# Kernel tuning notes

Hardware: AMD Instinct MI355X
Metric: run time of the kernel (lower is better)

## Reference

```python
import jax, jax.numpy as jnp
import numpy as np

EPS = 1e-5
NEG = -1e20


def layer_norm(x, gamma, beta):
    mu = jnp.mean(x, axis=-1, keepdims=True)
    var = jnp.mean(jnp.square(x - mu), axis=-1, keepdims=True)
    return (x - mu) * jax.lax.rsqrt(var + EPS) * gamma + beta


def setup_inputs() -> dict:
    key = jax.random.key(0)
    ks = jax.random.split(key, 12)
    B, S, D, H, HD = 2, 2048, 1024, 16, 64
    hid = H * HD
    inp = {
        "q": jax.random.normal(ks[0], (B, S, D), jnp.float32),
        "k": jax.random.normal(ks[1], (B, S, D), jnp.float32),
        "v": jax.random.normal(ks[2], (B, S, D), jnp.float32),
        "mask": jax.random.randint(ks[3], (B, 1, S, S), 0, 2, jnp.int32),
        "Wq": jax.random.normal(ks[4], (D, hid), jnp.float32) * (D ** -0.5),
        "bq": jnp.zeros((hid,), jnp.float32),
        "Wk": jax.random.normal(ks[5], (D, hid), jnp.float32) * (D ** -0.5),
        "bk": jnp.zeros((hid,), jnp.float32),
        "Wv": jax.random.normal(ks[6], (D, hid), jnp.float32) * (D ** -0.5),
        "bv": jnp.zeros((hid,), jnp.float32),
        "Wo": jax.random.normal(ks[7], (hid, D), jnp.float32) * (hid ** -0.5),
        "bo": jnp.zeros((D,), jnp.float32),
        "gamma": jnp.ones((D,), jnp.float32),
        "beta": jnp.zeros((D,), jnp.float32),
    }
    return inp


def reference(q, k, v, mask, Wq, bq, Wk, bk, Wv, bv, Wo, bo, gamma, beta):
    B, S, D = q.shape
    H, HD = 16, 64
    scale = HD ** -0.5
    qh = (layer_norm(q, gamma, beta) @ Wq + bq).reshape(B, S, H, HD).transpose(0, 2, 1, 3)
    kh = (layer_norm(k, gamma, beta) @ Wk + bk).reshape(B, S, H, HD).transpose(0, 2, 1, 3)
    vh = (layer_norm(v, gamma, beta) @ Wv + bv).reshape(B, S, H, HD).transpose(0, 2, 1, 3)
    dots = jnp.einsum('bhqd,bhkd->bhqk', qh, kh)  # [B,H,S,S]
    dots = jnp.where(mask == 0, NEG, dots) * scale  # mask BEFORE scale (as in source)
    attn = jax.nn.softmax(dots, axis=-1)
    out = jnp.einsum('bhqk,bhkd->bhqd', attn, vh)  # [B,H,S,HD]
    # Faithful to `out.view(B, S, -1)` on a [B,H,S,HD]-contiguous tensor: raw reshape,
    # no head transpose.
    out = out.reshape(B, S, H * HD)
    return out @ Wo + bo
```

## Files before the change

### kernel.cpp

```cpp
#include <hip/hip_runtime.h>

typedef short short8 __attribute__((ext_vector_type(8)));
typedef float f32x4 __attribute__((ext_vector_type(4)));

#define QSCALE 0.18033688011112042f

__device__ __forceinline__ unsigned short f2bf(float f) {
  unsigned u = __builtin_bit_cast(unsigned, f);
  u += 0x7fffu + ((u >> 16) & 1u);
  return (unsigned short)(u >> 16);
}

__device__ __forceinline__ void gload16(const void* g, void* l) {
  typedef __attribute__((address_space(1))) unsigned int gas;
  typedef __attribute__((address_space(3))) unsigned int las;
  __builtin_amdgcn_global_load_lds((gas*)(unsigned long long)g,
                                   (las*)(unsigned)(unsigned long long)l, 16, 0, 0);
}

__device__ __forceinline__ short8 mk8(unsigned r0, unsigned r1, unsigned r2, unsigned r3) {
  union { unsigned u[4]; short8 s; } t;
  t.u[0] = r0; t.u[1] = r1; t.u[2] = r2; t.u[3] = r3;
  return t.s;
}

#define MFMA16(a, b, c) __builtin_amdgcn_mfma_f32_16x16x32_bf16(a, b, c, 0, 0, 0)

__global__ __launch_bounds__(256) void wtrans_kernel(
    const float* __restrict__ Wq, const float* __restrict__ Wk,
    const float* __restrict__ Wv, const float* __restrict__ Wo,
    unsigned short* __restrict__ Wt) {
  const int wsel = blockIdx.z;
  const float* W = wsel == 0 ? Wq : wsel == 1 ? Wk : wsel == 2 ? Wv : Wo;
  const float wscale = (wsel == 0) ? QSCALE : 1.0f;
  unsigned short* out = Wt + (long)wsel * 1048576;
  __shared__ float lds[64][65];
  const int t = threadIdx.x;
  const int k0 = blockIdx.x * 64, n0 = blockIdx.y * 64;
#pragma unroll
  for (int i = 0; i < 4; ++i) {
    int r = (t >> 4) + i * 16, c4 = (t & 15) * 4;
    float4 vv = *(const float4*)(W + (long)(k0 + r) * 1024 + n0 + c4);
    lds[r][c4] = vv.x; lds[r][c4 + 1] = vv.y; lds[r][c4 + 2] = vv.z; lds[r][c4 + 3] = vv.w;
  }
  __syncthreads();
#pragma unroll
  for (int i = 0; i < 16; ++i) {
    int flat = t + i * 256;
    int n = flat >> 6, kk = flat & 63;
    out[(long)(n0 + n) * 1024 + k0 + kk] = f2bf(lds[kk][n] * wscale);
  }
}

__global__ __launch_bounds__(256) void maskpack_kernel(const int* __restrict__ mask,
                                                       unsigned* __restrict__ bits) {
  const long n = 8388608;
  const long stride = (long)gridDim.x * 256;
  const int lane = threadIdx.x & 63;
  for (long i = (long)blockIdx.x * 256 + threadIdx.x; i < n; i += stride) {
    unsigned long long bal = __ballot(mask[i] != 0);
    if ((lane & 31) == 0) bits[i >> 5] = (unsigned)(bal >> (lane & 32));
  }
}

__global__ __launch_bounds__(256) void ln_kernel(
    const float* __restrict__ q, const float* __restrict__ k, const float* __restrict__ v,
    const float* __restrict__ gamma, const float* __restrict__ beta,
    unsigned short* __restrict__ lnq, unsigned short* __restrict__ lnk,
    unsigned short* __restrict__ lnv) {
  const int row = blockIdx.x, which = blockIdx.y;
  const float* x = (which == 0 ? q : which == 1 ? k : v) + (long)row * 1024;
  unsigned short* y = (which == 0 ? lnq : which == 1 ? lnk : lnv) + (long)row * 1024;
  const int t = threadIdx.x, lane = t & 63, wv = t >> 6;
  float4 xv = ((const float4*)x)[t];
  float s = xv.x + xv.y + xv.z + xv.w;
  float s2 = xv.x * xv.x + xv.y * xv.y + xv.z * xv.z + xv.w * xv.w;
#pragma unroll
  for (int off = 32; off > 0; off >>= 1) {
    s += __shfl_down(s, off);
    s2 += __shfl_down(s2, off);
  }
  __shared__ float red[8];
  if (lane == 0) { red[wv] = s; red[wv + 4] = s2; }
  __syncthreads();
  float tot = red[0] + red[1] + red[2] + red[3];
  float tot2 = red[4] + red[5] + red[6] + red[7];
  float mu = tot * (1.0f / 1024.0f);
  float var = tot2 * (1.0f / 1024.0f) - mu * mu;
  float rs = rsqrtf(var + 1e-5f);
  float4 g = ((const float4*)gamma)[t];
  float4 be = ((const float4*)beta)[t];
  ushort4 o;
  o.x = f2bf((xv.x - mu) * rs * g.x + be.x);
  o.y = f2bf((xv.y - mu) * rs * g.y + be.y);
  o.z = f2bf((xv.z - mu) * rs * g.z + be.z);
  o.w = f2bf((xv.w - mu) * rs * g.w + be.w);
  ((ushort4*)y)[t] = o;
}

template <int BM, int MODE>
__global__ __launch_bounds__(256) void gemm_kernel(
    const unsigned short* __restrict__ A0, const unsigned short* __restrict__ A1,
    const unsigned short* __restrict__ A2, const unsigned short* __restrict__ Wt,
    const float* __restrict__ b0, const float* __restrict__ b1,
    const float* __restrict__ b2, unsigned short* __restrict__ outB,
    unsigned short* __restrict__ outV, float* __restrict__ outF) {
  constexpr int BK = 64;
  constexpr int MI = BM / 32;
  const int z = blockIdx.z;
  const unsigned short* A = z == 0 ? A0 : z == 1 ? A1 : A2;
  const unsigned short* Bt = Wt + (long)z * 1048576;
  const float* bias = z == 0 ? b0 : z == 1 ? b1 : b2;
  unsigned short* outz = outB + (long)z * 4194304;
  const float bscale = (MODE == 0 && z == 0) ? QSCALE : 1.0f;

  __shared__ char lds[BM * 128 + 16384];
  char* As = lds;
  char* Bs = lds + BM * 128;
  const int tid = threadIdx.x, lane = tid & 63, w = tid >> 6;
  const int wr = w >> 1, wc = w & 1;
  const int m0 = blockIdx.x * BM, n0 = blockIdx.y * 128;
  constexpr int K = 1024;
  constexpr int ACH = BM * 8 / 256;

  f32x4 acc[MI][4] = {};
  for (int kt = 0; kt < K / BK; ++kt) {
    __syncthreads();
#pragma unroll
    for (int i = 0; i < ACH; ++i) {
      int c = tid + i * 256;
      int row = c >> 3, pg = (c & 7) ^ (row & 7);
      gload16(A + (long)(m0 + row) * K + kt * BK + pg * 8, As + c * 16);
    }
#pragma unroll
    for (int i = 0; i < 4; ++i) {
      int c = tid + i * 256;
      int row = c >> 3, pg = (c & 7) ^ (row & 7);
      gload16(Bt + (long)(n0 + row) * K + kt * BK + pg * 8, Bs + c * 16);
    }
    asm volatile("s_waitcnt vmcnt(0)" ::: "memory");
    __syncthreads();
#pragma unroll
    for (int ks = 0; ks < 2; ++ks) {
      short8 af[MI], bf[4];
#pragma unroll
      for (int mi = 0; mi < MI; ++mi) {
        int row = wr * (BM / 2) + mi * 16 + (lane & 15);
        int part = (ks * 4 + (lane >> 4)) ^ (row & 7);
        af[mi] = *(const short8*)(As + row * 128 + part * 16);
      }
#pragma unroll
      for (int ni = 0; ni < 4; ++ni) {
        int row = wc * 64 + ni * 16 + (lane & 15);
        int part = (ks * 4 + (lane >> 4)) ^ (row & 7);
        bf[ni] = *(const short8*)(Bs + row * 128 + part * 16);
      }
#pragma unroll
      for (int mi = 0; mi < MI; ++mi)
#pragma unroll
        for (int ni = 0; ni < 4; ++ni)
          acc[mi][ni] = MFMA16(af[mi], bf[ni], acc[mi][ni]);
    }
  }
#pragma unroll
  for (int mi = 0; mi < MI; ++mi) {
    int mbase = m0 + wr * (BM / 2) + mi * 16 + ((lane >> 4) << 2);
#pragma unroll
    for (int ni = 0; ni < 4; ++ni) {
      int j = n0 + wc * 64 + ni * 16 + (lane & 15);
      float bj = bias[j] * bscale;
      float t0 = acc[mi][ni][0] + bj;
      float t1 = acc[mi][ni][1] + bj;
      float t2 = acc[mi][ni][2] + bj;
      float t3 = acc[mi][ni][3] + bj;
      if constexpr (MODE == 0) {
        int b = mbase >> 11, s = mbase & 2047;
        int h = j >> 6, d = j & 63;
        if (z == 2) {
          unsigned lo, hi;
          asm("v_cvt_pk_bf16_f32 %0, %1, %2" : "=v"(lo) : "v"(t0), "v"(t1));
          asm("v_cvt_pk_bf16_f32 %0, %1, %2" : "=v"(hi) : "v"(t2), "v"(t3));
          uint2 o; o.x = lo; o.y = hi;
          int sp = (s & ~31) | (((s >> 2) & 3) << 3) | (((s >> 4) & 1) << 2);
          *(uint2*)(outV + ((long)(b * 16 + h) * 64 + d) * 2048 + sp) = o;
        } else {
          long base = (((long)(b * 16 + h)) * 2048 + s) * 64 + d;
          outz[base] = f2bf(t0);
          outz[base + 64] = f2bf(t1);
          outz[base + 128] = f2bf(t2);
          outz[base + 192] = f2bf(t3);
        }
      } else {
        outF[(long)mbase * 1024 + j] = t0;
        outF[(long)(mbase + 1) * 1024 + j] = t1;
        outF[(long)(mbase + 2) * 1024 + j] = t2;
        outF[(long)(mbase + 3) * 1024 + j] = t3;
      }
    }
  }
}

__global__ __launch_bounds__(256, 4) void attn_kernel(
    const unsigned short* __restrict__ qh, const unsigned short* __restrict__ kh,
    const unsigned short* __restrict__ vt, const unsigned* __restrict__ mbits,
    unsigned short* __restrict__ O) {
  constexpr int S = 2048, NT = 32;
  __shared__ char lds[32768];
  char* Ks = lds;
  char* Vts = lds + 16384;
  const int tid = threadIdx.x, lane = tid & 63, w = tid >> 6;
  const int g = lane >> 4, c = lane & 15;

  const int flat = blockIdx.y * 32 + blockIdx.x;
  const int fl2 = (flat & 7) * 128 + (flat >> 3);
  const int qb = fl2 & 31, bh = fl2 >> 5, b = bh >> 4;
  const int kt0 = (fl2 & 3) * 8;

  const unsigned short* qp = qh + (long)bh * S * 64;
  const unsigned short* kp = kh + (long)bh * S * 64;
  const unsigned short* vp = vt + (long)bh * 64 * S;
  unsigned short* op = O + (long)bh * S * 64;
  const unsigned* mrow = mbits + (long)b * S * 64;
  const int q0 = qb * 64 + w * 16;
  const int myq = q0 + c;

  short8 bq_[2];
#pragma unroll
  for (int ds = 0; ds < 2; ++ds)
    bq_[ds] = *(const short8*)(qp + (long)myq * 64 + ds * 32 + g * 8);

  f32x4 o_acc[4] = {};
  float lpart = 0.f;

#define STAGE(KT, BUF)                                                              \
  {                                                                                 \
    _Pragma("unroll") for (int i = 0; i < 2; ++i) {                                 \
      int cc = tid + i * 256;                                                       \
      int row = cc >> 3, pg = (cc & 7) ^ (row & 7);                                 \
      gload16(kp + (long)((KT)*64 + row) * 64 + pg * 8, Ks + (BUF)*8192 + cc * 16); \
    }                                                                               \
    _Pragma("unroll") for (int i = 0; i < 2; ++i) {                                 \
      int cc = tid + i * 256;                                                       \
      int row = cc >> 3, pg = (cc & 7) ^ (row & 7);                                 \
      gload16(vp + (long)row * S + (KT)*64 + pg * 8, Vts + (BUF)*8192 + cc * 16);   \
    }                                                                               \
  }

  STAGE(kt0, 0);
  uint2 mcur = *(const uint2*)(mrow + (long)myq * 64 + kt0 * 2);
  uint2 mnxt = mcur;

  for (int kt = 0; kt < NT; ++kt) {
    const int cur = kt & 1;
    if (kt + 1 < NT) {
      const int nx = (kt0 + kt + 1) & 31;
      STAGE(nx, cur ^ 1);
      mnxt = *(const uint2*)(mrow + (long)myq * 64 + nx * 2);
      asm volatile("s_waitcnt vmcnt(5)" ::: "memory");
    } else {
      asm volatile("s_waitcnt vmcnt(0)" ::: "memory");
    }
    __builtin_amdgcn_s_barrier();

    f32x4 sc[4] = {};
    const char* Kb = Ks + cur * 8192;
    __builtin_amdgcn_s_setprio(1);
#pragma unroll
    for (int ds = 0; ds < 2; ++ds) {
#pragma unroll
      for (int kf = 0; kf < 4; ++kf) {
        int row = kf * 16 + c;
        int part = (ds * 4 + g) ^ (row & 7);
        short8 ak = *(const short8*)(Kb + row * 128 + part * 16);
        sc[kf] = MFMA16(ak, bq_[ds], sc[kf]);
      }
    }
    __builtin_amdgcn_s_setprio(0);

    unsigned ws0 = mcur.x >> (g * 4), ws1 = mcur.y >> (g * 4);
    unsigned pw[8];
#pragma unroll
    for (int kf = 0; kf < 4; ++kf) {
      unsigned wsh = ((kf >= 2) ? ws1 : ws0) >> ((kf & 1) * 16);
      float pv0 = __builtin_amdgcn_exp2f(sc[kf][0]);
      float pv1 = __builtin_amdgcn_exp2f(sc[kf][1]);
      float pv2 = __builtin_amdgcn_exp2f(sc[kf][2]);
      float pv3 = __builtin_amdgcn_exp2f(sc[kf][3]);
      pv0 = (wsh & 1u) ? pv0 : 0.f;
      pv1 = (wsh & 2u) ? pv1 : 0.f;
      pv2 = (wsh & 4u) ? pv2 : 0.f;
      pv3 = (wsh & 8u) ? pv3 : 0.f;
      lpart += (pv0 + pv1) + (pv2 + pv3);
      asm("v_cvt_pk_bf16_f32 %0, %1, %2" : "=v"(pw[kf * 2]) : "v"(pv0), "v"(pv1));
      asm("v_cvt_pk_bf16_f32 %0, %1, %2" : "=v"(pw[kf * 2 + 1]) : "v"(pv2), "v"(pv3));
    }
    short8 pa0 = mk8(pw[0], pw[1], pw[2], pw[3]);
    short8 pa1 = mk8(pw[4], pw[5], pw[6], pw[7]);
    mcur = mnxt;

    const char* Vb = Vts + cur * 8192;
    __builtin_amdgcn_s_setprio(1);
#pragma unroll
    for (int ks = 0; ks < 2; ++ks) {
      short8 pa = ks ? pa1 : pa0;
      int part = ks * 4 + g;
#pragma unroll
      for (int nd = 0; nd < 4; ++nd) {
        int d = nd * 16 + c;
        short8 bv = *(const short8*)(Vb + d * 128 + ((part ^ (d & 7)) * 16));
        o_acc[nd] = MFMA16(pa, bv, o_acc[nd]);
      }
    }
    __builtin_amdgcn_s_setprio(0);

    asm volatile("s_waitcnt lgkmcnt(0)" ::: "memory");
    __builtin_amdgcn_sched_barrier(0);
    __builtin_amdgcn_s_barrier();
  }
#undef STAGE

  lpart += __shfl_xor(lpart, 16);
  lpart += __shfl_xor(lpart, 32);
#pragma unroll
  for (int r = 0; r < 4; ++r) {
    float lr = __shfl(lpart, g * 4 + r);
    float inv = 1.0f / lr;
    int qrow = q0 + g * 4 + r;
#pragma unroll
    for (int nd = 0; nd < 4; ++nd)
      op[(long)qrow * 64 + nd * 16 + c] = f2bf(o_acc[nd][r] * inv);
  }
}

extern "C" void kernel_launch(void* const* d_in, const int* in_sizes, int n_in,
                              void* d_out, int out_size, void* d_ws, size_t ws_size,
                              hipStream_t stream) {
  const float* q = (const float*)d_in[0];
  const float* k = (const float*)d_in[1];
  const float* v = (const float*)d_in[2];
  const int* mask = (const int*)d_in[3];
  const float* Wq = (const float*)d_in[4];
  const float* bq = (const float*)d_in[5];
  const float* Wk = (const float*)d_in[6];
  const float* bk = (const float*)d_in[7];
  const float* Wv = (const float*)d_in[8];
  const float* bv = (const float*)d_in[9];
  const float* Wo = (const float*)d_in[10];
  const float* bo = (const float*)d_in[11];
  const float* gamma = (const float*)d_in[12];
  const float* beta = (const float*)d_in[13];
  float* out = (float*)d_out;

  char* ws = (char*)d_ws;
  unsigned short* Wt = (unsigned short*)ws;
  unsigned* mbits = (unsigned*)(ws + 8u * 1024 * 1024);
  unsigned short* lnq = (unsigned short*)(ws + 9u * 1024 * 1024);
  unsigned short* lnk = lnq + 4194304;
  unsigned short* lnv = lnk + 4194304;
  unsigned short* qh = lnv + 4194304;
  unsigned short* kh = qh + 4194304;
  unsigned short* vtb = kh + 4194304;
  unsigned short* Ob = lnq;

  wtrans_kernel<<<dim3(16, 16, 4), 256, 0, stream>>>(Wq, Wk, Wv, Wo, Wt);
  maskpack_kernel<<<1024, 256, 0, stream>>>(mask, mbits);
  ln_kernel<<<dim3(4096, 3), 256, 0, stream>>>(q, k, v, gamma, beta, lnq, lnk, lnv);
  gemm_kernel<128, 0><<<dim3(32, 8, 3), 256, 0, stream>>>(lnq, lnk, lnv, Wt, bq, bk, bv,
                                                          qh, vtb, nullptr);
  attn_kernel<<<dim3(32, 32), 256, 0, stream>>>(qh, kh, vtb, mbits, Ob);
  gemm_kernel<64, 1><<<dim3(64, 8, 1), 256, 0, stream>>>(Ob, Ob, Ob, Wt + 3 * 1048576,
                                                         bo, bo, bo, nullptr, nullptr, out);
}
```

Before: 149.2 us.

## Double-buffer GEMM LDS tiles with BK=32 and prefetch next stage

Restructures the projection GEMM main loop from a single-buffered BK=64 tile into a double-buffered BK=32 pipeline. The global-to-LDS loads for the next k-step are issued before the MFMAs on the current buffer, so load latency can overlap with compute. Only one barrier per iteration is kept, and s_setprio is raised around the MFMA block. The LDS swizzle is changed to fit the 64-byte rows. In exchange, smaller k-tiles double the number of iterations and barriers, and each step carries less MFMA work to hide latency.

```diff
diff --git a/kernel.cpp b/kernel.cpp
--- a/kernel.cpp
+++ b/kernel.cpp
@@ -105,8 +105,9 @@
     const float* __restrict__ b0, const float* __restrict__ b1,
     const float* __restrict__ b2, unsigned short* __restrict__ outB,
     unsigned short* __restrict__ outV, float* __restrict__ outF) {
-  constexpr int BK = 64;
   constexpr int MI = BM / 32;
+  constexpr int NT = 32;
+  constexpr int ACHA = BM / 64;
   const int z = blockIdx.z;
   const unsigned short* A = z == 0 ? A0 : z == 1 ? A1 : A2;
   const unsigned short* Bt = Wt + (long)z * 1048576;
@@ -114,54 +115,66 @@
   unsigned short* outz = outB + (long)z * 4194304;
   const float bscale = (MODE == 0 && z == 0) ? QSCALE : 1.0f;
 
-  __shared__ char lds[BM * 128 + 16384];
+  __shared__ char lds[(BM + 128) * 128];
   char* As = lds;
   char* Bs = lds + BM * 128;
   const int tid = threadIdx.x, lane = tid & 63, w = tid >> 6;
+  const int g = lane >> 4;
   const int wr = w >> 1, wc = w & 1;
   const int m0 = blockIdx.x * BM, n0 = blockIdx.y * 128;
-  constexpr int K = 1024;
-  constexpr int ACH = BM * 8 / 256;
 
   f32x4 acc[MI][4] = {};
-  for (int kt = 0; kt < K / BK; ++kt) {
-    __syncthreads();
-#pragma unroll
-    for (int i = 0; i < ACH; ++i) {
-      int c = tid + i * 256;
-      int row = c >> 3, pg = (c & 7) ^ (row & 7);
-      gload16(A + (long)(m0 + row) * K + kt * BK + pg * 8, As + c * 16);
-    }
-#pragma unroll
-    for (int i = 0; i < 4; ++i) {
-      int c = tid + i * 256;
-      int row = c >> 3, pg = (c & 7) ^ (row & 7);
-      gload16(Bt + (long)(n0 + row) * K + kt * BK + pg * 8, Bs + c * 16);
-    }
-    asm volatile("s_waitcnt vmcnt(0)" ::: "memory");
-    __syncthreads();
-#pragma unroll
-    for (int ks = 0; ks < 2; ++ks) {
-      short8 af[MI], bf[4];
-#pragma unroll
-      for (int mi = 0; mi < MI; ++mi) {
-        int row = wr * (BM / 2) + mi * 16 + (lane & 15);
-        int part = (ks * 4 + (lane >> 4)) ^ (row & 7);
-        af[mi] = *(const short8*)(As + row * 128 + part * 16);
-      }
-#pragma unroll
-      for (int ni = 0; ni < 4; ++ni) {
-        int row = wc * 64 + ni * 16 + (lane & 15);
-        int part = (ks * 4 + (lane >> 4)) ^ (row & 7);
-        bf[ni] = *(const short8*)(Bs + row * 128 + part * 16);
-      }
-#pragma unroll
-      for (int mi = 0; mi < MI; ++mi)
-#pragma unroll
-        for (int ni = 0; ni < 4; ++ni)
-          acc[mi][ni] = MFMA16(af[mi], bf[ni], acc[mi][ni]);
-    }
-  }
+
+#define GSTAGE(KT, BUF)                                                       \
+  {                                                                           \
+    _Pragma("unroll") for (int i = 0; i < ACHA; ++i) {                        \
+      int cc = tid + i * 256;                                                 \
+      int row = cc >> 2, p = cc & 3;                                          \
+      int kk = p ^ ((row >> 1) & 3);                                          \
+      gload16(A + (long)(m0 + row) * 1024 + (KT)*32 + kk * 8,                 \
+              As + (BUF) * (BM * 64) + cc * 16);                              \
+    }                                                                         \
+    _Pragma("unroll") for (int i = 0; i < 2; ++i) {                           \
+      int cc = tid + i * 256;                                                 \
+      int row = cc >> 2, p = cc & 3;                                          \
+      int kk = p ^ ((row >> 1) & 3);                                          \
+      gload16(Bt + (long)(n0 + row) * 1024 + (KT)*32 + kk * 8,                \
+              Bs + (BUF)*8192 + cc * 16);                                     \
+    }                                                                         \
+  }
+
+  GSTAGE(0, 0);
+  asm volatile("s_waitcnt vmcnt(0)" ::: "memory");
+  __builtin_amdgcn_s_barrier();
+
+  for (int kt = 0; kt < NT; ++kt) {
+    const int cur = kt & 1;
+    if (kt + 1 < NT) GSTAGE(kt + 1, cur ^ 1);
+    short8 af[MI], bf[4];
+#pragma unroll
+    for (int mi = 0; mi < MI; ++mi) {
+      int row = wr * (BM / 2) + mi * 16 + (lane & 15);
+      int part = g ^ ((row >> 1) & 3);
+      af[mi] = *(const short8*)(As + cur * (BM * 64) + row * 64 + part * 16);
+    }
+#pragma unroll
+    for (int ni = 0; ni < 4; ++ni) {
+      int row = wc * 64 + ni * 16 + (lane & 15);
+      int part = g ^ ((row >> 1) & 3);
+      bf[ni] = *(const short8*)(Bs + cur * 8192 + row * 64 + part * 16);
+    }
+    __builtin_amdgcn_s_setprio(1);
+#pragma unroll
+    for (int mi = 0; mi < MI; ++mi)
+#pragma unroll
+      for (int ni = 0; ni < 4; ++ni)
+        acc[mi][ni] = MFMA16(af[mi], bf[ni], acc[mi][ni]);
+    __builtin_amdgcn_s_setprio(0);
+    asm volatile("s_waitcnt vmcnt(0) lgkmcnt(0)" ::: "memory");
+    __builtin_amdgcn_s_barrier();
+  }
+#undef GSTAGE
+
 #pragma unroll
   for (int mi = 0; mi < MI; ++mi) {
     int mbase = m0 + wr * (BM / 2) + mi * 16 + ((lane >> 4) << 2);
```

Result: faster. 142.6 us (-4.4%).
